# Performance work log

Measured on AMD Instinct MI355X. Metric: run time of the kernel, lower is better.

## Reference

```python
import jax, jax.numpy as jnp
import numpy as np

D_MODEL = 256
NHEAD = 4
K_MODE = 8


def setup_inputs() -> dict:
    key = jax.random.key(0)
    ks = jax.random.split(key, 12)
    bs, S = 2, 4096
    inp = {
        "q": jax.random.normal(ks[0], (bs, S, D_MODEL), jnp.float32),
        "k": jax.random.normal(ks[1], (bs, S, D_MODEL + K_MODE), jnp.float32),
        "v": jax.random.normal(ks[2], (bs, S, D_MODEL), jnp.float32),
        "mask": jax.random.randint(ks[3], (bs, S, S), 0, 2, jnp.int32),
        # nn.Linear params: W is [out, in], y = x @ W.T + b
        "Wq": jax.random.normal(ks[4], (D_MODEL, D_MODEL), jnp.float32) * 0.02,
        "bq": jnp.zeros((D_MODEL,), jnp.float32),
        "Wk": jax.random.normal(ks[5], (D_MODEL, D_MODEL + K_MODE), jnp.float32) * 0.02,
        "bk": jnp.zeros((D_MODEL,), jnp.float32),
        "Wv": jax.random.normal(ks[6], (D_MODEL, D_MODEL), jnp.float32) * 0.02,
        "bv": jnp.zeros((D_MODEL,), jnp.float32),
        "Wo": jax.random.normal(ks[7], (D_MODEL, NHEAD * D_MODEL), jnp.float32) * 0.02,
        "bo": jnp.zeros((D_MODEL,), jnp.float32),
    }
    return inp


def reference(q, k, v, mask, Wq, bq, Wk, bk, Wv, bv, Wo, bo):
    # Projections (nn.Linear: x @ W.T + b). In the original module the projected
    # q/k/v are repeat-broadcast identically across all nhead heads (d_k = d_model),
    # and the mask broadcasts across heads too (dropout disabled). Hence every head
    # computes the exact same attention output; we compute it once and tile the
    # concat, which is mathematically identical and avoids redundant HBM traffic.
    qh = jnp.einsum('bsd,ed->bse', q, Wq) + bq   # [bs, S, d]
    kh = jnp.einsum('bsd,ed->bse', k, Wk) + bk   # [bs, S, d]
    vh = jnp.einsum('bsd,ed->bse', v, Wv) + bv   # [bs, S, d]

    scale = 1.0 / jnp.sqrt(jnp.asarray(D_MODEL, qh.dtype))
    scores = jnp.einsum('bqd,bkd->bqk', qh, kh) * scale  # [bs, S, S]
    scores = jnp.where(mask == 0, jnp.asarray(-1e9, scores.dtype), scores)
    attn = jax.nn.softmax(scores, axis=-1)
    per_head = jnp.einsum('bqk,bkd->bqd', attn, vh)      # [bs, S, d]

    concat = jnp.tile(per_head, (1, 1, NHEAD))           # [bs, S, h*d]
    return jnp.einsum('bsf,df->bsd', concat, Wo) + bo
```

## Files before the change

kernel.cpp:

```cpp
#include <hip/hip_runtime.h>

typedef unsigned short u16;
typedef unsigned int u32;
typedef __bf16 bf16x8 __attribute__((ext_vector_type(8)));
typedef float f32x4 __attribute__((ext_vector_type(4)));

#define S_LEN 4096
#define DM 256

__device__ __forceinline__ u16 f2b(float f) {
  u32 u = __builtin_bit_cast(u32, f);
  u = (u + 0x7FFFu + ((u >> 16) & 1u)) >> 16;
  return (u16)u;
}
__device__ __forceinline__ float b2f(u16 b) {
  return __builtin_bit_cast(float, (u32)b << 16);
}

__device__ __forceinline__ f32x4 mfma16(bf16x8 a, bf16x8 b, f32x4 c) {
  return __builtin_amdgcn_mfma_f32_16x16x32_bf16(a, b, c, 0, 0, 0);
}

template <int TIN_F32, int TOUT_F32, int BIAS_MODE>
__global__ __launch_bounds__(256, 2) void gemm_nt_kernel(
    const void* __restrict__ Ap, const void* __restrict__ Bp,
    void* __restrict__ Cp, const float* __restrict__ bias, float scale,
    int M, int N, int K, int lda, int ldb, int ldc,
    long sA, long sB, long sC) {
  __shared__ u16 As[64][72];
  __shared__ u16 Bs[64][72];
  const int tid = threadIdx.x;
  const int w = tid >> 6, ln = tid & 63, lg = ln >> 4, ll = ln & 15;
  const int m0 = blockIdx.x * 64, n0 = blockIdx.y * 64;
  const long zA = (long)blockIdx.z * sA, zB = (long)blockIdx.z * sB,
             zC = (long)blockIdx.z * sC;

  const f32x4 fzero = {0.f, 0.f, 0.f, 0.f};
  f32x4 acc[4];
#pragma unroll
  for (int i = 0; i < 4; ++i) acc[i] = fzero;

  const int srow = tid >> 2, scb = (tid & 3) * 16;
  const int nk = (K + 63) >> 6;
  for (int kc = 0; kc < nk; ++kc) {
    const int k0 = kc * 64;
    if (TIN_F32) {
      {
        const float* src = (const float*)Ap + zA + (size_t)(m0 + srow) * lda + k0 + scb;
        u16 t[16];
        if (k0 + 64 <= K) {
#pragma unroll
          for (int i = 0; i < 16; ++i) t[i] = f2b(src[i]);
        } else {
#pragma unroll
          for (int i = 0; i < 16; ++i) {
            int gk = k0 + scb + i;
            t[i] = (gk < K) ? f2b(src[i]) : (u16)0;
          }
        }
#pragma unroll
        for (int i = 0; i < 16; ++i) As[srow][scb + i] = t[i];
      }
      {
        const float* src = (const float*)Bp + zB + (size_t)(n0 + srow) * ldb + k0 + scb;
        u16 t[16];
        if (k0 + 64 <= K) {
#pragma unroll
          for (int i = 0; i < 16; ++i) t[i] = f2b(src[i]);
        } else {
#pragma unroll
          for (int i = 0; i < 16; ++i) {
            int gk = k0 + scb + i;
            t[i] = (gk < K) ? f2b(src[i]) : (u16)0;
          }
        }
#pragma unroll
        for (int i = 0; i < 16; ++i) Bs[srow][scb + i] = t[i];
      }
    } else {
      const u16* srcA = (const u16*)Ap + zA + (size_t)(m0 + srow) * lda + k0 + scb;
      *(bf16x8*)&As[srow][scb] = *(const bf16x8*)srcA;
      *(bf16x8*)&As[srow][scb + 8] = *(const bf16x8*)(srcA + 8);
      const u16* srcB = (const u16*)Bp + zB + (size_t)(n0 + srow) * ldb + k0 + scb;
      *(bf16x8*)&Bs[srow][scb] = *(const bf16x8*)srcB;
      *(bf16x8*)&Bs[srow][scb + 8] = *(const bf16x8*)(srcB + 8);
    }
    __syncthreads();
#pragma unroll
    for (int ks = 0; ks < 2; ++ks) {
      bf16x8 af = *(const bf16x8*)&As[w * 16 + ll][ks * 32 + lg * 8];
#pragma unroll
      for (int ct = 0; ct < 4; ++ct) {
        bf16x8 bfr = *(const bf16x8*)&Bs[ct * 16 + ll][ks * 32 + lg * 8];
        acc[ct] = mfma16(af, bfr, acc[ct]);
      }
    }
    __syncthreads();
  }

#pragma unroll
  for (int ct = 0; ct < 4; ++ct) {
#pragma unroll
    for (int j = 0; j < 4; ++j) {
      int row = m0 + w * 16 + lg * 4 + j;
      int col = n0 + ct * 16 + ll;
      float v = acc[ct][j];
      if (BIAS_MODE == 1) v += bias[col];
      if (BIAS_MODE == 2) v += bias[row];
      v *= scale;
      if (TOUT_F32)
        ((float*)Cp)[zC + (size_t)row * ldc + col] = v;
      else
        ((u16*)Cp)[zC + (size_t)row * ldc + col] = f2b(v);
    }
  }
}

__global__ void wos_kernel(const float* __restrict__ Wo, u16* __restrict__ WoS) {
  int d = blockIdx.x, e = threadIdx.x;
  const float* p = Wo + (size_t)d * 1024;
  WoS[(size_t)d * 256 + e] = f2b(p[e] + p[256 + e] + p[512 + e] + p[768 + e]);
}

__global__ __launch_bounds__(512, 4) void flash_kernel(
    const u16* __restrict__ qh, const u16* __restrict__ kh,
    const u16* __restrict__ vhT, const int* __restrict__ mask,
    u16* __restrict__ Opart, float* __restrict__ Lpart) {
  __shared__ u16 kh_s[32 * 256];
  __shared__ u16 vs_s[256 * 32];
  __shared__ u16 p_s[8][16][40];

  const int tid = threadIdx.x;
  const int w = tid >> 6, ln = tid & 63, lg = ln >> 4, ll = ln & 15;
  const int q0 = blockIdx.x * 128;
  const int b = blockIdx.y;
  const int h = blockIdx.z;

  bf16x8 qf[8];
  {
    const u16* qp = qh + (size_t)(b * S_LEN + q0 + w * 16 + ll) * DM + lg * 8;
#pragma unroll
    for (int ks = 0; ks < 8; ++ks) qf[ks] = *(const bf16x8*)(qp + ks * 32);
  }

  const f32x4 fzero = {0.f, 0.f, 0.f, 0.f};
  f32x4 acc_o[16];
#pragma unroll
  for (int i = 0; i < 16; ++i) acc_o[i] = fzero;
  float l_run[4] = {0.f, 0.f, 0.f, 0.f};

  const u16* kbase = kh + (size_t)(b * S_LEN + h * 512) * DM;
  const u16* vbase = vhT + (size_t)b * DM * S_LEN + h * 512;
  const int* mbase = mask + (size_t)(b * S_LEN + q0 + w * 16) * S_LEN + h * 512;

  for (int t = 0; t < 16; ++t) {
#pragma unroll
    for (int i = 0; i < 2; ++i) {
      int c = i * 512 + tid;
      int row = c >> 5, cc = c & 31;
      bf16x8 val = *(const bf16x8*)(kbase + (size_t)(t * 32 + row) * DM + cc * 8);
      *(bf16x8*)&kh_s[row * 256 + ((cc ^ (row & 7)) << 3)] = val;
    }
#pragma unroll
    for (int i = 0; i < 2; ++i) {
      int c = i * 512 + tid;
      int row = c >> 2, cc = c & 3;
      bf16x8 val = *(const bf16x8*)(vbase + (size_t)row * S_LEN + t * 32 + cc * 8);
      *(bf16x8*)&vs_s[row * 32 + ((cc ^ ((row >> 1) & 3)) << 3)] = val;
    }
    __syncthreads();

    int mv0[4], mv1[4];
#pragma unroll
    for (int j = 0; j < 4; ++j) {
      const int* mr = mbase + (size_t)(lg * 4 + j) * S_LEN + t * 32;
      mv0[j] = mr[ll];
      mv1[j] = mr[16 + ll];
    }

    f32x4 accs0 = fzero, accs1 = fzero;
#pragma unroll
    for (int ks = 0; ks < 8; ++ks) {
      const int cc = ks * 4 + lg;
      bf16x8 kf0 = *(const bf16x8*)&kh_s[ll * 256 + ((cc ^ (ll & 7)) << 3)];
      accs0 = mfma16(qf[ks], kf0, accs0);
      bf16x8 kf1 = *(const bf16x8*)&kh_s[(16 + ll) * 256 + ((cc ^ (ll & 7)) << 3)];
      accs1 = mfma16(qf[ks], kf1, accs1);
    }

    float p0[4], p1[4];
#pragma unroll
    for (int j = 0; j < 4; ++j) {
      p0[j] = mv0[j] ? __expf(accs0[j]) : 0.f;
      p1[j] = mv1[j] ? __expf(accs1[j]) : 0.f;
      l_run[j] += p0[j] + p1[j];
    }
#pragma unroll
    for (int j = 0; j < 4; ++j) {
      int r = lg * 4 + j;
      p_s[w][r][ll] = f2b(p0[j]);
      p_s[w][r][16 + ll] = f2b(p1[j]);
    }
    bf16x8 pf = *(const bf16x8*)&p_s[w][ll][lg * 8];

#pragma unroll
    for (int dt = 0; dt < 16; ++dt) {
      int vrow = dt * 16 + ll;
      bf16x8 vf = *(const bf16x8*)&vs_s[vrow * 32 + ((lg ^ ((vrow >> 1) & 3)) << 3)];
      acc_o[dt] = mfma16(pf, vf, acc_o[dt]);
    }
    __syncthreads();
  }

#pragma unroll
  for (int j = 0; j < 4; ++j) {
    l_run[j] += __shfl_xor(l_run[j], 1);
    l_run[j] += __shfl_xor(l_run[j], 2);
    l_run[j] += __shfl_xor(l_run[j], 4);
    l_run[j] += __shfl_xor(l_run[j], 8);
  }
  const size_t growb = (size_t)h * 8192 + (size_t)b * S_LEN + q0 + w * 16;
  if (ll == 0) {
#pragma unroll
    for (int j = 0; j < 4; ++j) Lpart[growb + lg * 4 + j] = l_run[j];
  }
#pragma unroll
  for (int dt = 0; dt < 16; ++dt) {
#pragma unroll
    for (int j = 0; j < 4; ++j) {
      Opart[(growb + lg * 4 + j) * 256 + dt * 16 + ll] = f2b(acc_o[dt][j]);
    }
  }
}

__global__ void combine_kernel(const u16* __restrict__ Opart,
                               const float* __restrict__ Lpart,
                               u16* __restrict__ ph) {
  const int r = blockIdx.x;
  const int d = threadIdx.x;
  float o = 0.f, l = 0.f;
#pragma unroll
  for (int s = 0; s < 8; ++s) {
    l += Lpart[(size_t)s * 8192 + r];
    o += b2f(Opart[((size_t)s * 8192 + r) * 256 + d]);
  }
  ph[(size_t)r * 256 + d] = f2b(o / l);
}

extern "C" void kernel_launch(void* const* d_in, const int* in_sizes, int n_in,
                              void* d_out, int out_size, void* d_ws, size_t ws_size,
                              hipStream_t stream) {
  const float* q = (const float*)d_in[0];
  const float* k = (const float*)d_in[1];
  const float* v = (const float*)d_in[2];
  const int* mask = (const int*)d_in[3];
  const float* Wq = (const float*)d_in[4];
  const float* bq = (const float*)d_in[5];
  const float* Wk = (const float*)d_in[6];
  const float* bk = (const float*)d_in[7];
  const float* Wv = (const float*)d_in[8];
  const float* bv = (const float*)d_in[9];
  const float* Wo = (const float*)d_in[10];
  const float* bo = (const float*)d_in[11];

  char* ws = (char*)d_ws;
  u16* qh = (u16*)(ws + 0);
  u16* kh = (u16*)(ws + 4194304);
  u16* vhT = (u16*)(ws + 8388608);
  u16* WoS = (u16*)(ws + 12582912);
  u16* ph = (u16*)(ws + 12713984);
  u16* Op = (u16*)(ws + 16908288);
  float* Lp = (float*)(ws + 50462720);

  dim3 blk(256);
  gemm_nt_kernel<1, 0, 1><<<dim3(128, 4, 1), blk, 0, stream>>>(
      q, Wq, qh, bq, 0.0625f, 8192, 256, 256, 256, 256, 256, 0, 0, 0);
  gemm_nt_kernel<1, 0, 1><<<dim3(128, 4, 1), blk, 0, stream>>>(
      k, Wk, kh, bk, 1.0f, 8192, 256, 264, 264, 264, 256, 0, 0, 0);
  gemm_nt_kernel<1, 0, 2><<<dim3(4, 64, 2), blk, 0, stream>>>(
      Wv, v, vhT, bv, 1.0f, 256, 4096, 256, 256, 256, 4096,
      0, (long)4096 * 256, (long)256 * 4096);
  wos_kernel<<<dim3(256), blk, 0, stream>>>(Wo, WoS);
  flash_kernel<<<dim3(32, 2, 8), dim3(512), 0, stream>>>(qh, kh, vhT, mask, Op, Lp);
  combine_kernel<<<dim3(8192), blk, 0, stream>>>(Op, Lp, ph);
  gemm_nt_kernel<0, 1, 1><<<dim3(128, 4, 1), blk, 0, stream>>>(
      ph, WoS, d_out, bo, 1.0f, 8192, 256, 256, 256, 256, 256, 0, 0, 0);
}
```

Baseline: 152.0 us.

## Bitpack mask, double-buffer K/V via direct global-to-LDS loads, 32 rows per wave

Adds a pre-pass that packs the int32 mask into bits with wave ballots, so the flash kernel reads one u32 per row per tile instead of 32 ints. The flash kernel now uses 256 threads, each wave handling 32 query rows so each K/V fragment feeds two MFMAs. K/V tiles are double-buffered and loaded with global_load_lds, overlapping the next tile's fetch with compute. The bitpack kernel still reads the full mask once, and the larger per-wave register set may lower occupancy. qh's workspace is reused for the combine output.

```diff
diff --git a/kernel.cpp b/kernel.cpp
--- a/kernel.cpp
+++ b/kernel.cpp
@@ -2,6 +2,7 @@
 
 typedef unsigned short u16;
 typedef unsigned int u32;
+typedef unsigned long long u64;
 typedef __bf16 bf16x8 __attribute__((ext_vector_type(8)));
 typedef float f32x4 __attribute__((ext_vector_type(4)));
 
@@ -19,6 +20,12 @@
 
 __device__ __forceinline__ f32x4 mfma16(bf16x8 a, bf16x8 b, f32x4 c) {
   return __builtin_amdgcn_mfma_f32_16x16x32_bf16(a, b, c, 0, 0, 0);
+}
+
+__device__ __forceinline__ void gl_lds16(const u16* g, u16* l) {
+  __builtin_amdgcn_global_load_lds(
+      (const __attribute__((address_space(1))) u32*)g,
+      (__attribute__((address_space(3))) u32*)l, 16, 0, 0);
 }
 
 template <int TIN_F32, int TOUT_F32, int BIAS_MODE>
@@ -122,13 +129,33 @@
   WoS[(size_t)d * 256 + e] = f2b(p[e] + p[256 + e] + p[512 + e] + p[768 + e]);
 }
 
-__global__ __launch_bounds__(512, 4) void flash_kernel(
+__global__ __launch_bounds__(256) void bitpack_kernel(const int* __restrict__ mask,
+                                                      u32* __restrict__ mb) {
+  const int ln = threadIdx.x & 63;
+  const int gw = (int)((blockIdx.x * 256 + threadIdx.x) >> 6);
+  const int nw = gridDim.x * 4;
+  u64* mb64 = (u64*)mb;
+  for (int it = gw; it < 131072; it += nw) {
+    const int* p = mask + (size_t)it * 256 + ln;
+    int v0 = p[0], v1 = p[64], v2 = p[128], v3 = p[192];
+    u64 b0 = __ballot(v0 != 0);
+    u64 b1 = __ballot(v1 != 0);
+    u64 b2 = __ballot(v2 != 0);
+    u64 b3 = __ballot(v3 != 0);
+    if (ln < 4) {
+      u64 val = ln == 0 ? b0 : (ln == 1 ? b1 : (ln == 2 ? b2 : b3));
+      mb64[(size_t)it * 4 + ln] = val;
+    }
+  }
+}
+
+__global__ __launch_bounds__(256, 2) void flash_kernel(
     const u16* __restrict__ qh, const u16* __restrict__ kh,
-    const u16* __restrict__ vhT, const int* __restrict__ mask,
+    const u16* __restrict__ vhT, const u32* __restrict__ mb,
     u16* __restrict__ Opart, float* __restrict__ Lpart) {
-  __shared__ u16 kh_s[32 * 256];
-  __shared__ u16 vs_s[256 * 32];
-  __shared__ u16 p_s[8][16][40];
+  __shared__ u16 kh_s[2][32 * 256];
+  __shared__ u16 vs_s[2][256 * 32];
+  __shared__ u16 p_s[4][32][40];
 
   const int tid = threadIdx.x;
   const int w = tid >> 6, ln = tid & 63, lg = ln >> 4, ll = ln & 15;
@@ -136,101 +163,130 @@
   const int b = blockIdx.y;
   const int h = blockIdx.z;
 
-  bf16x8 qf[8];
-  {
-    const u16* qp = qh + (size_t)(b * S_LEN + q0 + w * 16 + ll) * DM + lg * 8;
-#pragma unroll
-    for (int ks = 0; ks < 8; ++ks) qf[ks] = *(const bf16x8*)(qp + ks * 32);
+  bf16x8 qf[2][8];
+#pragma unroll
+  for (int qg = 0; qg < 2; ++qg) {
+    const u16* qp = qh + (size_t)(b * S_LEN + q0 + w * 32 + qg * 16 + ll) * DM + lg * 8;
+#pragma unroll
+    for (int ks = 0; ks < 8; ++ks) qf[qg][ks] = *(const bf16x8*)(qp + ks * 32);
   }
 
   const f32x4 fzero = {0.f, 0.f, 0.f, 0.f};
-  f32x4 acc_o[16];
-#pragma unroll
-  for (int i = 0; i < 16; ++i) acc_o[i] = fzero;
-  float l_run[4] = {0.f, 0.f, 0.f, 0.f};
+  f32x4 acc_o[2][16];
+#pragma unroll
+  for (int qg = 0; qg < 2; ++qg)
+#pragma unroll
+    for (int i = 0; i < 16; ++i) acc_o[qg][i] = fzero;
+  float l_run[2][4] = {{0.f, 0.f, 0.f, 0.f}, {0.f, 0.f, 0.f, 0.f}};
 
   const u16* kbase = kh + (size_t)(b * S_LEN + h * 512) * DM;
   const u16* vbase = vhT + (size_t)b * DM * S_LEN + h * 512;
-  const int* mbase = mask + (size_t)(b * S_LEN + q0 + w * 16) * S_LEN + h * 512;
-
+  const u32* mbase = mb + (size_t)(b * S_LEN + q0 + w * 32) * 128 + h * 16;
+
+  auto stage = [&](int t, int buf) {
+#pragma unroll
+    for (int i = 0; i < 4; ++i) {
+      int c = i * 256 + tid;
+      int row = c >> 5, ccl = c & 31;
+      int ccg = ccl ^ (row & 7);
+      gl_lds16(kbase + (size_t)(t * 32 + row) * DM + ccg * 8,
+               &kh_s[buf][(i * 256 + w * 64) * 8]);
+    }
+#pragma unroll
+    for (int i = 0; i < 4; ++i) {
+      int c = i * 256 + tid;
+      int row = c >> 2, cc = c & 3;
+      gl_lds16(vbase + (size_t)row * S_LEN + t * 32 + cc * 8,
+               &vs_s[buf][(i * 256 + w * 64) * 8]);
+    }
+  };
+
+  stage(0, 0);
+  __syncthreads();
+
+  int cur = 0;
   for (int t = 0; t < 16; ++t) {
-#pragma unroll
-    for (int i = 0; i < 2; ++i) {
-      int c = i * 512 + tid;
-      int row = c >> 5, cc = c & 31;
-      bf16x8 val = *(const bf16x8*)(kbase + (size_t)(t * 32 + row) * DM + cc * 8);
-      *(bf16x8*)&kh_s[row * 256 + ((cc ^ (row & 7)) << 3)] = val;
-    }
-#pragma unroll
-    for (int i = 0; i < 2; ++i) {
-      int c = i * 512 + tid;
-      int row = c >> 2, cc = c & 3;
-      bf16x8 val = *(const bf16x8*)(vbase + (size_t)row * S_LEN + t * 32 + cc * 8);
-      *(bf16x8*)&vs_s[row * 32 + ((cc ^ ((row >> 1) & 3)) << 3)] = val;
-    }
-    __syncthreads();
-
-    int mv0[4], mv1[4];
-#pragma unroll
-    for (int j = 0; j < 4; ++j) {
-      const int* mr = mbase + (size_t)(lg * 4 + j) * S_LEN + t * 32;
-      mv0[j] = mr[ll];
-      mv1[j] = mr[16 + ll];
-    }
-
-    f32x4 accs0 = fzero, accs1 = fzero;
+    u32 mw[2][4];
+#pragma unroll
+    for (int qg = 0; qg < 2; ++qg)
+#pragma unroll
+      for (int j = 0; j < 4; ++j)
+        mw[qg][j] = mbase[(size_t)(qg * 16 + lg * 4 + j) * 128 + t];
+
+    if (t + 1 < 16) stage(t + 1, cur ^ 1);
+
+    f32x4 accs[2][2];
+    accs[0][0] = fzero;
+    accs[0][1] = fzero;
+    accs[1][0] = fzero;
+    accs[1][1] = fzero;
 #pragma unroll
     for (int ks = 0; ks < 8; ++ks) {
-      const int cc = ks * 4 + lg;
-      bf16x8 kf0 = *(const bf16x8*)&kh_s[ll * 256 + ((cc ^ (ll & 7)) << 3)];
-      accs0 = mfma16(qf[ks], kf0, accs0);
-      bf16x8 kf1 = *(const bf16x8*)&kh_s[(16 + ll) * 256 + ((cc ^ (ll & 7)) << 3)];
-      accs1 = mfma16(qf[ks], kf1, accs1);
-    }
-
-    float p0[4], p1[4];
-#pragma unroll
-    for (int j = 0; j < 4; ++j) {
-      p0[j] = mv0[j] ? __expf(accs0[j]) : 0.f;
-      p1[j] = mv1[j] ? __expf(accs1[j]) : 0.f;
-      l_run[j] += p0[j] + p1[j];
-    }
-#pragma unroll
-    for (int j = 0; j < 4; ++j) {
-      int r = lg * 4 + j;
-      p_s[w][r][ll] = f2b(p0[j]);
-      p_s[w][r][16 + ll] = f2b(p1[j]);
-    }
-    bf16x8 pf = *(const bf16x8*)&p_s[w][ll][lg * 8];
+#pragma unroll
+      for (int half = 0; half < 2; ++half) {
+        int krow = half * 16 + ll;
+        bf16x8 kf = *(const bf16x8*)&kh_s[cur][krow * 256 +
+                                              (((ks * 4 + lg) ^ (krow & 7)) << 3)];
+        accs[0][half] = mfma16(qf[0][ks], kf, accs[0][half]);
+        accs[1][half] = mfma16(qf[1][ks], kf, accs[1][half]);
+      }
+    }
+
+#pragma unroll
+    for (int qg = 0; qg < 2; ++qg) {
+#pragma unroll
+      for (int j = 0; j < 4; ++j) {
+        u32 m = mw[qg][j];
+        float p0 = ((m >> ll) & 1u) ? __expf(accs[qg][0][j]) : 0.f;
+        float p1 = ((m >> (16 + ll)) & 1u) ? __expf(accs[qg][1][j]) : 0.f;
+        l_run[qg][j] += p0 + p1;
+        int r = qg * 16 + lg * 4 + j;
+        p_s[w][r][ll] = f2b(p0);
+        p_s[w][r][16 + ll] = f2b(p1);
+      }
+    }
+    bf16x8 pf0 = *(const bf16x8*)&p_s[w][ll][lg * 8];
+    bf16x8 pf1 = *(const bf16x8*)&p_s[w][16 + ll][lg * 8];
 
 #pragma unroll
     for (int dt = 0; dt < 16; ++dt) {
       int vrow = dt * 16 + ll;
-      bf16x8 vf = *(const bf16x8*)&vs_s[vrow * 32 + ((lg ^ ((vrow >> 1) & 3)) << 3)];
-      acc_o[dt] = mfma16(pf, vf, acc_o[dt]);
+      bf16x8 vf = *(const bf16x8*)&vs_s[cur][vrow * 32 + lg * 8];
+      acc_o[0][dt] = mfma16(pf0, vf, acc_o[0][dt]);
+      acc_o[1][dt] = mfma16(pf1, vf, acc_o[1][dt]);
     }
     __syncthreads();
-  }
-
-#pragma unroll
-  for (int j = 0; j < 4; ++j) {
-    l_run[j] += __shfl_xor(l_run[j], 1);
-    l_run[j] += __shfl_xor(l_run[j], 2);
-    l_run[j] += __shfl_xor(l_run[j], 4);
-    l_run[j] += __shfl_xor(l_run[j], 8);
-  }
-  const size_t growb = (size_t)h * 8192 + (size_t)b * S_LEN + q0 + w * 16;
+    cur ^= 1;
+  }
+
+#pragma unroll
+  for (int qg = 0; qg < 2; ++qg) {
+#pragma unroll
+    for (int j = 0; j < 4; ++j) {
+      float l = l_run[qg][j];
+      l += __shfl_xor(l, 1);
+      l += __shfl_xor(l, 2);
+      l += __shfl_xor(l, 4);
+      l += __shfl_xor(l, 8);
+      l_run[qg][j] = l;
+    }
+  }
+  const size_t growb = (size_t)h * 8192 + (size_t)b * S_LEN + q0 + w * 32;
   if (ll == 0) {
 #pragma unroll
-    for (int j = 0; j < 4; ++j) Lpart[growb + lg * 4 + j] = l_run[j];
-  }
-#pragma unroll
-  for (int dt = 0; dt < 16; ++dt) {
-#pragma unroll
-    for (int j = 0; j < 4; ++j) {
-      Opart[(growb + lg * 4 + j) * 256 + dt * 16 + ll] = f2b(acc_o[dt][j]);
-    }
-  }
+    for (int qg = 0; qg < 2; ++qg)
+#pragma unroll
+      for (int j = 0; j < 4; ++j)
+        Lpart[growb + qg * 16 + lg * 4 + j] = l_run[qg][j];
+  }
+#pragma unroll
+  for (int qg = 0; qg < 2; ++qg)
+#pragma unroll
+    for (int dt = 0; dt < 16; ++dt)
+#pragma unroll
+      for (int j = 0; j < 4; ++j)
+        Opart[(growb + qg * 16 + lg * 4 + j) * 256 + dt * 16 + ll] =
+            f2b(acc_o[qg][dt][j]);
 }
 
 __global__ void combine_kernel(const u16* __restrict__ Opart,
@@ -268,7 +324,7 @@
   u16* kh = (u16*)(ws + 4194304);
   u16* vhT = (u16*)(ws + 8388608);
   u16* WoS = (u16*)(ws + 12582912);
-  u16* ph = (u16*)(ws + 12713984);
+  u32* mb = (u32*)(ws + 12713984);
   u16* Op = (u16*)(ws + 16908288);
   float* Lp = (float*)(ws + 50462720);
 
@@ -281,8 +337,9 @@
       Wv, v, vhT, bv, 1.0f, 256, 4096, 256, 256, 256, 4096,
       0, (long)4096 * 256, (long)256 * 4096);
   wos_kernel<<<dim3(256), blk, 0, stream>>>(Wo, WoS);
-  flash_kernel<<<dim3(32, 2, 8), dim3(512), 0, stream>>>(qh, kh, vhT, mask, Op, Lp);
-  combine_kernel<<<dim3(8192), blk, 0, stream>>>(Op, Lp, ph);
+  bitpack_kernel<<<dim3(2048), blk, 0, stream>>>(mask, mb);
+  flash_kernel<<<dim3(32, 2, 8), blk, 0, stream>>>(qh, kh, vhT, mb, Op, Lp);
+  combine_kernel<<<dim3(8192), blk, 0, stream>>>(Op, Lp, qh);
   gemm_nt_kernel<0, 1, 1><<<dim3(128, 4, 1), blk, 0, stream>>>(
-      ph, WoS, d_out, bo, 1.0f, 8192, 256, 256, 256, 256, 256, 0, 0, 0);
-}
+      qh, WoS, d_out, bo, 1.0f, 8192, 256, 256, 256, 256, 256, 0, 0, 0);
+}
```

Result: faster. 133.4 us (-12.3%).
